# Kernel optimization log

Measured on AMD Instinct MI355X. Metric: run time of the kernel, lower is better.

## Reference

```python
import jax, jax.numpy as jnp
import numpy as np

N = 1_000_000      # particles
K = 27             # 3x3x3 stencil taps
C_IN = 16
C_OUT = 4
NSTENCILS = 3


def setup_inputs() -> dict:
    key = jax.random.key(0)
    k1, k2, k3, k4 = jax.random.split(key, 4)
    x = jax.random.normal(k1, (N, C_IN), dtype=jnp.float32)
    W = jax.random.normal(k2, (NSTENCILS, K, C_IN, C_OUT), dtype=jnp.float32) * (1.0 / np.sqrt(K * C_IN))
    aprs = jax.random.randint(k3, (N, K), 0, N, dtype=jnp.int64)
    level_deltas = jax.random.randint(k4, (N,), 0, NSTENCILS, dtype=jnp.int64)
    return {"x": x, "W": W, "aprs": aprs, "level_deltas": level_deltas}


def reference(x, W, aprs, level_deltas):
    # Irregular neighbor gather: [N, K, C_in]
    gathered = x[aprs]
    # Level-dependent stencil contraction + select (nstencils is tiny, loop is over stencils not data)
    out = jnp.zeros((x.shape[0], W.shape[-1]), dtype=x.dtype)
    for s in range(NSTENCILS):
        contrib = jnp.einsum('nkc,kcd->nd', gathered, W[s])  # [N, C_out]
        out = jnp.where((level_deltas == s)[:, None], contrib, out)
    # Unfused final activation (nn.ReLU in OutBlock)
    return jax.nn.relu(out)
```

## Files before the change

### kernel.cpp

```cpp
#include <hip/hip_runtime.h>

constexpr int K    = 27;
constexpr int CIN  = 16;
constexpr int COUT = 4;
constexpr int NS   = 3;
constexpr int WSZ  = K * CIN * COUT;
constexpr int WPAD = WSZ + 8;

constexpr int NCH  = 32;
constexpr int CHSH = 15;
constexpr int NPL  = 4;
constexpr int NPW  = 256;
constexpr int RNDS = K * NPL;
constexpr int EPW  = RNDS * 64;
constexpr unsigned int SENT = 0xFFFFFFFFu;
constexpr int WREG = 34;

typedef unsigned int uint;
typedef float  f32x4 __attribute__((ext_vector_type(4)));
typedef uint   u32x4 __attribute__((ext_vector_type(4)));
typedef uint   u32x2 __attribute__((ext_vector_type(2)));
typedef _Float16 h16x2 __attribute__((ext_vector_type(2)));

__device__ __forceinline__ uint pkh(float lo, float hi) {
    union { h16x2 h; uint u; } v;
    v.h.x = (_Float16)lo; v.h.y = (_Float16)hi;
    return v.u;
}
__device__ __forceinline__ h16x2 u2h(uint u) {
    union { uint u; h16x2 h; } v; v.u = u; return v.h;
}

#if defined(__has_builtin)
#if __has_builtin(__builtin_amdgcn_fdot2)
#define HAVE_FDOT2 1
#endif
#endif

__device__ __forceinline__ float dot2acc(uint xp, uint wp, float acc) {
#ifdef HAVE_FDOT2
    return __builtin_amdgcn_fdot2(u2h(xp), u2h(wp), acc, false);
#else
    const h16x2 a = u2h(xp), b = u2h(wp);
    acc = fmaf((float)a.x, (float)b.x, acc);
    return fmaf((float)a.y, (float)b.y, acc);
#endif
}

__device__ __forceinline__ uint bf16_rne(float f) {
    uint u = __float_as_uint(f);
    u += 0x7FFFu + ((u >> 16) & 1u);
    return u >> 16;
}
__device__ __forceinline__ float blo(uint u) { return __uint_as_float(u << 16); }
__device__ __forceinline__ float bhi(uint u) { return __uint_as_float(u & 0xFFFF0000u); }

__global__ __launch_bounds__(256) void cvt_f16(
    const float* __restrict__ x, uint* __restrict__ xh, int nvec)
{
    int i = blockIdx.x * 256 + threadIdx.x;
    if (i >= nvec) return;
    const f32x4* xf = reinterpret_cast<const f32x4*>(x) + 2 * (size_t)i;
    f32x4 a = __builtin_nontemporal_load(&xf[0]);
    f32x4 b = __builtin_nontemporal_load(&xf[1]);
    u32x4 o;
    o.x = pkh(a.x, a.y);
    o.y = pkh(a.z, a.w);
    o.z = pkh(b.x, b.y);
    o.w = pkh(b.z, b.w);
    __builtin_nontemporal_store(o, &reinterpret_cast<u32x4*>(xh)[i]);
}

__global__ __launch_bounds__(64) void bucket_kernel(
    const int* __restrict__ aprs,
    const int* __restrict__ lvl,
    uint* __restrict__ ent,
    int n)
{
    __shared__ uint stage[EPW];
    __shared__ int  posL[NCH * 64];

    const int w    = blockIdx.x;
    const int lane = threadIdx.x;
    const int i0   = w * NPW + lane * NPL;
    const int* __restrict__ ap = aprs + (size_t)i0 * K;

    #pragma unroll
    for (int c = 0; c < NCH; ++c) posL[c * 64 + lane] = 0;
    for (int t = 0; t < RNDS; ++t) stage[t * 64 + lane] = SENT;

    for (int b = 0; b < NPL; ++b) {
        if (i0 + b < n) {
            for (int j = 0; j < K; ++j) {
                const int ch = (int)(((uint)ap[b * K + j]) >> CHSH);
                posL[ch * 64 + lane] += 1;
            }
        }
    }
    int run = 0;
    #pragma unroll
    for (int c = 0; c < NCH; ++c) {
        const int cc = posL[c * 64 + lane];
        posL[c * 64 + lane] = run;
        run += cc;
    }
    for (int b = 0; b < NPL; ++b) {
        if (i0 + b < n) {
            const uint s = (uint)lvl[i0 + b];
            const uint tag = ((uint)b << 7) | (s << 5);
            for (int j = 0; j < K; ++j) {
                const uint nb = (uint)ap[b * K + j];
                const int ch  = (int)(nb >> CHSH);
                const int slot = posL[ch * 64 + lane];
                posL[ch * 64 + lane] = slot + 1;
                stage[slot * 64 + lane] = (nb << 9) | tag | (uint)j;
            }
        }
    }
    uint* __restrict__ eb = ent + (size_t)w * EPW;
    for (int t = 0; t < RNDS; ++t) eb[t * 64 + lane] = stage[t * 64 + lane];
}

__global__ __launch_bounds__(256, 4) void compute_kernel(
    const uint*  __restrict__ xh,
    const float* __restrict__ Wg,
    const uint*  __restrict__ ent,
    float*       __restrict__ out,
    int n)
{
    __shared__ __align__(8) uint Wb[NS * K * WREG];

    const int tid = threadIdx.x;
    for (int idx = tid; idx < NS * K * 32; idx += 256) {
        const int reg = idx >> 5, g = idx & 31;
        const int q = g >> 3, p = g & 7;
        Wb[reg * WREG + g] = pkh(Wg[reg * 64 + 8 * p + q],
                                 Wg[reg * 64 + 8 * p + 4 + q]);
    }
    __syncthreads();

    const int widx = tid >> 6, lane = tid & 63;
    const int w = blockIdx.x * 4 + widx;
    const uint* __restrict__ eb = ent + (size_t)w * EPW;

    f32x4 A0 = {0,0,0,0}, A1 = {0,0,0,0}, A2 = {0,0,0,0}, A3 = {0,0,0,0};

    uint eC  = eb[lane];
    uint eN  = eb[64 + lane];
    uint eN2 = eb[128 + lane];
    {
        const uint nbC = (eC == SENT) ? 0u : (eC >> 9);
        const u32x4* __restrict__ xrC =
            reinterpret_cast<const u32x4*>(xh + (size_t)nbC * 8);
        u32x4 xC0 = xrC[0];
        u32x4 xC1 = xrC[1];
        const uint nbN = (eN == SENT) ? 0u : (eN >> 9);
        const u32x4* __restrict__ xrN =
            reinterpret_cast<const u32x4*>(xh + (size_t)nbN * 8);
        u32x4 xN0 = xrN[0];
        u32x4 xN1 = xrN[1];

        for (int s = 0; s < RNDS; ++s) {
            const int sF = (s + 3 < RNDS) ? s + 3 : RNDS - 1;
            const uint eF = eb[(size_t)sF * 64 + lane];
            const uint nb2 = (eN2 == SENT) ? 0u : (eN2 >> 9);
            const u32x4* __restrict__ xr2 =
                reinterpret_cast<const u32x4*>(xh + (size_t)nb2 * 8);
            const u32x4 x20 = xr2[0];
            const u32x4 x21 = xr2[1];

            const bool valid = (eC != SENT);
            const uint bq  = (eC >> 7) & 3u;
            const uint skr = ((eC >> 5) & 3u) * (uint)K + (eC & 31u);
            const uint sk  = valid ? skr : 0u;
            const uint* __restrict__ wr = &Wb[sk * WREG];

            uint xd[8];
            xd[0] = xC0.x; xd[1] = xC0.y; xd[2] = xC0.z; xd[3] = xC0.w;
            xd[4] = xC1.x; xd[5] = xC1.y; xd[6] = xC1.z; xd[7] = xC1.w;

            float pq0 = 0.f, pq1 = 0.f, pq2 = 0.f, pq3 = 0.f;
            #pragma unroll
            for (int t = 0; t < 4; ++t) {
                const u32x2 w0 = *reinterpret_cast<const u32x2*>(wr +  0 + 2 * t);
                const u32x2 w1 = *reinterpret_cast<const u32x2*>(wr +  8 + 2 * t);
                const u32x2 w2 = *reinterpret_cast<const u32x2*>(wr + 16 + 2 * t);
                const u32x2 w3 = *reinterpret_cast<const u32x2*>(wr + 24 + 2 * t);
                pq0 = dot2acc(xd[2 * t], w0.x, pq0);
                pq0 = dot2acc(xd[2 * t + 1], w0.y, pq0);
                pq1 = dot2acc(xd[2 * t], w1.x, pq1);
                pq1 = dot2acc(xd[2 * t + 1], w1.y, pq1);
                pq2 = dot2acc(xd[2 * t], w2.x, pq2);
                pq2 = dot2acc(xd[2 * t + 1], w2.y, pq2);
                pq3 = dot2acc(xd[2 * t], w3.x, pq3);
                pq3 = dot2acc(xd[2 * t + 1], w3.y, pq3);
            }
            const float m0 = (valid && bq == 0u) ? 1.f : 0.f;
            const float m1 = (valid && bq == 1u) ? 1.f : 0.f;
            const float m2 = (valid && bq == 2u) ? 1.f : 0.f;
            const float m3 = (valid && bq == 3u) ? 1.f : 0.f;
            A0.x = fmaf(m0, pq0, A0.x); A0.y = fmaf(m0, pq1, A0.y);
            A0.z = fmaf(m0, pq2, A0.z); A0.w = fmaf(m0, pq3, A0.w);
            A1.x = fmaf(m1, pq0, A1.x); A1.y = fmaf(m1, pq1, A1.y);
            A1.z = fmaf(m1, pq2, A1.z); A1.w = fmaf(m1, pq3, A1.w);
            A2.x = fmaf(m2, pq0, A2.x); A2.y = fmaf(m2, pq1, A2.y);
            A2.z = fmaf(m2, pq2, A2.z); A2.w = fmaf(m2, pq3, A2.w);
            A3.x = fmaf(m3, pq0, A3.x); A3.y = fmaf(m3, pq1, A3.y);
            A3.z = fmaf(m3, pq2, A3.z); A3.w = fmaf(m3, pq3, A3.w);

            eC = eN;  xC0 = xN0; xC1 = xN1;
            eN = eN2; xN0 = x20; xN1 = x21;
            eN2 = eF;
        }
    }

    const int i0 = w * NPW + lane * NPL;
    f32x4* __restrict__ op = reinterpret_cast<f32x4*>(out);
    f32x4 o;
    if (i0 + 0 < n) {
        o.x = fmaxf(A0.x,0.f); o.y = fmaxf(A0.y,0.f); o.z = fmaxf(A0.z,0.f); o.w = fmaxf(A0.w,0.f);
        __builtin_nontemporal_store(o, op + i0 + 0);
    }
    if (i0 + 1 < n) {
        o.x = fmaxf(A1.x,0.f); o.y = fmaxf(A1.y,0.f); o.z = fmaxf(A1.z,0.f); o.w = fmaxf(A1.w,0.f);
        __builtin_nontemporal_store(o, op + i0 + 1);
    }
    if (i0 + 2 < n) {
        o.x = fmaxf(A2.x,0.f); o.y = fmaxf(A2.y,0.f); o.z = fmaxf(A2.z,0.f); o.w = fmaxf(A2.w,0.f);
        __builtin_nontemporal_store(o, op + i0 + 2);
    }
    if (i0 + 3 < n) {
        o.x = fmaxf(A3.x,0.f); o.y = fmaxf(A3.y,0.f); o.z = fmaxf(A3.z,0.f); o.w = fmaxf(A3.w,0.f);
        __builtin_nontemporal_store(o, op + i0 + 3);
    }
}

__global__ __launch_bounds__(256) void cvt_bf16(
    const float* __restrict__ x, uint* __restrict__ xh, int nvec)
{
    int i = blockIdx.x * 256 + threadIdx.x;
    if (i >= nvec) return;
    const f32x4* xf = reinterpret_cast<const f32x4*>(x) + 2 * (size_t)i;
    f32x4 a = __builtin_nontemporal_load(&xf[0]);
    f32x4 b = __builtin_nontemporal_load(&xf[1]);
    u32x4 o;
    o.x = bf16_rne(a.x) | (bf16_rne(a.y) << 16);
    o.y = bf16_rne(a.z) | (bf16_rne(a.w) << 16);
    o.z = bf16_rne(b.x) | (bf16_rne(b.y) << 16);
    o.w = bf16_rne(b.z) | (bf16_rne(b.w) << 16);
    __builtin_nontemporal_store(o, &reinterpret_cast<u32x4*>(xh)[i]);
}

__global__ __launch_bounds__(256) void outblock_bf16(
    const uint*  __restrict__ xh,
    const float* __restrict__ W,
    const int*   __restrict__ aprs,
    const int*   __restrict__ lvl,
    float*       __restrict__ out,
    int n)
{
    __shared__ float Wl[NS * WPAD];
    for (int i = threadIdx.x; i < NS * WSZ; i += 256) {
        int s = i / WSZ;
        Wl[s * WPAD + (i - s * WSZ)] = W[i];
    }
    __syncthreads();

    int nIdx = blockIdx.x * 256 + threadIdx.x;
    if (nIdx >= n) return;

    const int s = lvl[nIdx];
    const float* __restrict__ Ws = &Wl[s * WPAD];
    const int*   __restrict__ ap = aprs + (size_t)nIdx * K;

    float a0 = 0.f, a1 = 0.f, a2 = 0.f, a3 = 0.f;
    #pragma unroll 3
    for (int k = 0; k < K; ++k) {
        const int nb = ap[k];
        const u32x4* __restrict__ xr =
            reinterpret_cast<const u32x4*>(xh + (size_t)nb * 8);
        const u32x4 p0 = xr[0];
        const u32x4 p1 = xr[1];
        const float* __restrict__ Wk = Ws + k * (CIN * COUT);
        float xv[16];
        xv[ 0] = blo(p0.x); xv[ 1] = bhi(p0.x);
        xv[ 2] = blo(p0.y); xv[ 3] = bhi(p0.y);
        xv[ 4] = blo(p0.z); xv[ 5] = bhi(p0.z);
        xv[ 6] = blo(p0.w); xv[ 7] = bhi(p0.w);
        xv[ 8] = blo(p1.x); xv[ 9] = bhi(p1.x);
        xv[10] = blo(p1.y); xv[11] = bhi(p1.y);
        xv[12] = blo(p1.z); xv[13] = bhi(p1.z);
        xv[14] = blo(p1.w); xv[15] = bhi(p1.w);
        #pragma unroll
        for (int cq = 0; cq < CIN; ++cq) {
            const float4 wv = *reinterpret_cast<const float4*>(&Wk[cq * COUT]);
            a0 = fmaf(xv[cq], wv.x, a0);
            a1 = fmaf(xv[cq], wv.y, a1);
            a2 = fmaf(xv[cq], wv.z, a2);
            a3 = fmaf(xv[cq], wv.w, a3);
        }
    }
    f32x4 o;
    o.x = fmaxf(a0, 0.f); o.y = fmaxf(a1, 0.f);
    o.z = fmaxf(a2, 0.f); o.w = fmaxf(a3, 0.f);
    __builtin_nontemporal_store(o, reinterpret_cast<f32x4*>(out) + nIdx);
}

__global__ __launch_bounds__(256) void outblock_f32(
    const float* __restrict__ x,
    const float* __restrict__ W,
    const int*   __restrict__ aprs,
    const int*   __restrict__ lvl,
    float*       __restrict__ out,
    int n)
{
    __shared__ float Wl[NS * WPAD];
    for (int i = threadIdx.x; i < NS * WSZ; i += 256) {
        int s = i / WSZ;
        Wl[s * WPAD + (i - s * WSZ)] = W[i];
    }
    __syncthreads();
    int nIdx = blockIdx.x * 256 + threadIdx.x;
    if (nIdx >= n) return;
    const int s = lvl[nIdx];
    const float* __restrict__ Ws = &Wl[s * WPAD];
    const int*   __restrict__ ap = aprs + (size_t)nIdx * K;
    float a0 = 0.f, a1 = 0.f, a2 = 0.f, a3 = 0.f;
    #pragma unroll 3
    for (int k = 0; k < K; ++k) {
        const int nb = ap[k];
        const float4* __restrict__ xr =
            reinterpret_cast<const float4*>(x + (size_t)nb * CIN);
        const float4 v0 = xr[0], v1 = xr[1], v2 = xr[2], v3 = xr[3];
        const float* __restrict__ Wk = Ws + k * (CIN * COUT);
        float xv[16];
        xv[ 0] = v0.x; xv[ 1] = v0.y; xv[ 2] = v0.z; xv[ 3] = v0.w;
        xv[ 4] = v1.x; xv[ 5] = v1.y; xv[ 6] = v1.z; xv[ 7] = v1.w;
        xv[ 8] = v2.x; xv[ 9] = v2.y; xv[10] = v2.z; xv[11] = v2.w;
        xv[12] = v3.x; xv[13] = v3.y; xv[14] = v3.z; xv[15] = v3.w;
        #pragma unroll
        for (int cq = 0; cq < CIN; ++cq) {
            const float4 wv = *reinterpret_cast<const float4*>(&Wk[cq * COUT]);
            a0 = fmaf(xv[cq], wv.x, a0);
            a1 = fmaf(xv[cq], wv.y, a1);
            a2 = fmaf(xv[cq], wv.z, a2);
            a3 = fmaf(xv[cq], wv.w, a3);
        }
    }
    float4 o;
    o.x = fmaxf(a0, 0.f); o.y = fmaxf(a1, 0.f);
    o.z = fmaxf(a2, 0.f); o.w = fmaxf(a3, 0.f);
    reinterpret_cast<float4*>(out)[nIdx] = o;
}

extern "C" void kernel_launch(void* const* d_in, const int* in_sizes, int n_in,
                              void* d_out, int out_size, void* d_ws, size_t ws_size,
                              hipStream_t stream) {
    const float* x    = (const float*)d_in[0];
    const float* W    = (const float*)d_in[1];
    const int*   aprs = (const int*)d_in[2];
    const int*   lvl  = (const int*)d_in[3];
    float*       out  = (float*)d_out;

    const int n = in_sizes[0] / CIN;

    const int nwaves    = (n + NPW - 1) / NPW;
    const int nblocks   = (nwaves + 3) / 4;
    const int nwavesPad = nblocks * 4;

    const size_t xhB  = (size_t)n * CIN * 2;
    const size_t entB = (size_t)nwavesPad * EPW * 4;
    const size_t needChunked = xhB + entB;

    if (ws_size >= needChunked && n <= (1 << 20)) {
        uint* xh  = (uint*)d_ws;
        uint* ent = (uint*)((char*)d_ws + xhB);
        const int nvec = n * CIN / 8;
        cvt_f16<<<(nvec + 255) / 256, 256, 0, stream>>>(x, xh, nvec);
        bucket_kernel<<<nwavesPad, 64, 0, stream>>>(aprs, lvl, ent, n);
        compute_kernel<<<nblocks, 256, 0, stream>>>(xh, W, ent, out, n);
    } else if (ws_size >= xhB) {
        uint* xh = (uint*)d_ws;
        const int nvec = n * CIN / 8;
        cvt_bf16<<<(nvec + 255) / 256, 256, 0, stream>>>(x, xh, nvec);
        outblock_bf16<<<(n + 255) / 256, 256, 0, stream>>>(xh, W, aprs, lvl, out, n);
    } else {
        outblock_f32<<<(n + 255) / 256, 256, 0, stream>>>(x, W, aprs, lvl, out, n);
    }
}
```

Baseline: 307.0 us.

## Deepen gather prefetch pipeline and shrink compute blocks to two waves

The compute kernel's software pipeline now keeps three gathered x rows in flight instead of two, with the entry index fetched four rounds ahead, to hide more random-gather latency. The block size also drops from four waves to two, with the launch and workspace padding adjusted to match. This adds register pressure for the extra in-flight vectors. Smaller blocks mean each block reloads the shared-memory weight table for fewer waves, so that staging cost is amortised less.

```diff
diff --git a/kernel.cpp b/kernel.cpp
--- a/kernel.cpp
+++ b/kernel.cpp
@@ -15,6 +15,7 @@
 constexpr int EPW  = RNDS * 64;
 constexpr unsigned int SENT = 0xFFFFFFFFu;
 constexpr int WREG = 34;
+constexpr int BWAV = 2;
 
 typedef unsigned int uint;
 typedef float  f32x4 __attribute__((ext_vector_type(4)));
@@ -121,7 +122,7 @@
     for (int t = 0; t < RNDS; ++t) eb[t * 64 + lane] = stage[t * 64 + lane];
 }
 
-__global__ __launch_bounds__(256, 4) void compute_kernel(
+__global__ __launch_bounds__(BWAV * 64, 4) void compute_kernel(
     const uint*  __restrict__ xh,
     const float* __restrict__ Wg,
     const uint*  __restrict__ ent,
@@ -131,7 +132,7 @@
     __shared__ __align__(8) uint Wb[NS * K * WREG];
 
     const int tid = threadIdx.x;
-    for (int idx = tid; idx < NS * K * 32; idx += 256) {
+    for (int idx = tid; idx < NS * K * 32; idx += BWAV * 64) {
         const int reg = idx >> 5, g = idx & 31;
         const int q = g >> 3, p = g & 7;
         Wb[reg * WREG + g] = pkh(Wg[reg * 64 + 8 * p + q],
@@ -140,44 +141,50 @@
     __syncthreads();
 
     const int widx = tid >> 6, lane = tid & 63;
-    const int w = blockIdx.x * 4 + widx;
+    const int w = blockIdx.x * BWAV + widx;
     const uint* __restrict__ eb = ent + (size_t)w * EPW;
 
     f32x4 A0 = {0,0,0,0}, A1 = {0,0,0,0}, A2 = {0,0,0,0}, A3 = {0,0,0,0};
 
-    uint eC  = eb[lane];
-    uint eN  = eb[64 + lane];
-    uint eN2 = eb[128 + lane];
+    uint e0 = eb[lane];
+    uint e1 = eb[64 + lane];
+    uint e2 = eb[128 + lane];
+    uint e3 = eb[192 + lane];
     {
-        const uint nbC = (eC == SENT) ? 0u : (eC >> 9);
-        const u32x4* __restrict__ xrC =
-            reinterpret_cast<const u32x4*>(xh + (size_t)nbC * 8);
-        u32x4 xC0 = xrC[0];
-        u32x4 xC1 = xrC[1];
-        const uint nbN = (eN == SENT) ? 0u : (eN >> 9);
-        const u32x4* __restrict__ xrN =
-            reinterpret_cast<const u32x4*>(xh + (size_t)nbN * 8);
-        u32x4 xN0 = xrN[0];
-        u32x4 xN1 = xrN[1];
+        const uint nb0 = (e0 == SENT) ? 0u : (e0 >> 9);
+        const u32x4* __restrict__ xr0 =
+            reinterpret_cast<const u32x4*>(xh + (size_t)nb0 * 8);
+        u32x4 X0a = xr0[0];
+        u32x4 X0b = xr0[1];
+        const uint nb1 = (e1 == SENT) ? 0u : (e1 >> 9);
+        const u32x4* __restrict__ xr1 =
+            reinterpret_cast<const u32x4*>(xh + (size_t)nb1 * 8);
+        u32x4 X1a = xr1[0];
+        u32x4 X1b = xr1[1];
+        const uint nb2 = (e2 == SENT) ? 0u : (e2 >> 9);
+        const u32x4* __restrict__ xr2 =
+            reinterpret_cast<const u32x4*>(xh + (size_t)nb2 * 8);
+        u32x4 X2a = xr2[0];
+        u32x4 X2b = xr2[1];
 
         for (int s = 0; s < RNDS; ++s) {
-            const int sF = (s + 3 < RNDS) ? s + 3 : RNDS - 1;
+            const int sF = (s + 4 < RNDS) ? s + 4 : RNDS - 1;
             const uint eF = eb[(size_t)sF * 64 + lane];
-            const uint nb2 = (eN2 == SENT) ? 0u : (eN2 >> 9);
-            const u32x4* __restrict__ xr2 =
-                reinterpret_cast<const u32x4*>(xh + (size_t)nb2 * 8);
-            const u32x4 x20 = xr2[0];
-            const u32x4 x21 = xr2[1];
-
-            const bool valid = (eC != SENT);
-            const uint bq  = (eC >> 7) & 3u;
-            const uint skr = ((eC >> 5) & 3u) * (uint)K + (eC & 31u);
+            const uint nb3 = (e3 == SENT) ? 0u : (e3 >> 9);
+            const u32x4* __restrict__ xr3 =
+                reinterpret_cast<const u32x4*>(xh + (size_t)nb3 * 8);
+            const u32x4 X3a = xr3[0];
+            const u32x4 X3b = xr3[1];
+
+            const bool valid = (e0 != SENT);
+            const uint bq  = (e0 >> 7) & 3u;
+            const uint skr = ((e0 >> 5) & 3u) * (uint)K + (e0 & 31u);
             const uint sk  = valid ? skr : 0u;
             const uint* __restrict__ wr = &Wb[sk * WREG];
 
             uint xd[8];
-            xd[0] = xC0.x; xd[1] = xC0.y; xd[2] = xC0.z; xd[3] = xC0.w;
-            xd[4] = xC1.x; xd[5] = xC1.y; xd[6] = xC1.z; xd[7] = xC1.w;
+            xd[0] = X0a.x; xd[1] = X0a.y; xd[2] = X0a.z; xd[3] = X0a.w;
+            xd[4] = X0b.x; xd[5] = X0b.y; xd[6] = X0b.z; xd[7] = X0b.w;
 
             float pq0 = 0.f, pq1 = 0.f, pq2 = 0.f, pq3 = 0.f;
             #pragma unroll
@@ -208,9 +215,10 @@
             A3.x = fmaf(m3, pq0, A3.x); A3.y = fmaf(m3, pq1, A3.y);
             A3.z = fmaf(m3, pq2, A3.z); A3.w = fmaf(m3, pq3, A3.w);
 
-            eC = eN;  xC0 = xN0; xC1 = xN1;
-            eN = eN2; xN0 = x20; xN1 = x21;
-            eN2 = eF;
+            e0 = e1; X0a = X1a; X0b = X1b;
+            e1 = e2; X1a = X2a; X1b = X2b;
+            e2 = e3; X2a = X3a; X2b = X3b;
+            e3 = eF;
         }
     }
 
@@ -365,8 +373,8 @@
     const int n = in_sizes[0] / CIN;
 
     const int nwaves    = (n + NPW - 1) / NPW;
-    const int nblocks   = (nwaves + 3) / 4;
-    const int nwavesPad = nblocks * 4;
+    const int nblocks   = (nwaves + BWAV - 1) / BWAV;
+    const int nwavesPad = nblocks * BWAV;
 
     const size_t xhB  = (size_t)n * CIN * 2;
     const size_t entB = (size_t)nwavesPad * EPW * 4;
@@ -378,7 +386,7 @@
         const int nvec = n * CIN / 8;
         cvt_f16<<<(nvec + 255) / 256, 256, 0, stream>>>(x, xh, nvec);
         bucket_kernel<<<nwavesPad, 64, 0, stream>>>(aprs, lvl, ent, n);
-        compute_kernel<<<nblocks, 256, 0, stream>>>(xh, W, ent, out, n);
+        compute_kernel<<<nblocks, BWAV * 64, 0, stream>>>(xh, W, ent, out, n);
     } else if (ws_size >= xhB) {
         uint* xh = (uint*)d_ws;
         const int nvec = n * CIN / 8;
```

Result: slower. 351.0 us (+14.3%).
